# Kernel optimization log

Hardware: AMD Instinct MI355X
Metric: run time of the kernel (lower is better)

Reference implementation:

```python
import jax, jax.numpy as jnp
import numpy as np

B, N, N_MELS = 8, 4096, 64
DIM, LAYERS, HEADS = 256, 4, 4
DIM_HEAD = DIM // HEADS      # 64
INNER = HEADS * DIM_HEAD     # 256
NB_FEAT = 256                # random features
FF_MULT = 4                  # performer_pytorch FeedForward default


def _ortho_projection(rows, cols, rng):
    # gaussian_orthogonal_random_matrix, scaling=0 (performer_pytorch default)
    blocks = []
    for _ in range((rows + cols - 1) // cols):
        q, _ = np.linalg.qr(rng.standard_normal((cols, cols)))
        blocks.append(q.T)
    mat = np.concatenate(blocks)[:rows]
    multiplier = np.linalg.norm(rng.standard_normal((rows, cols)), axis=1)
    return (mat * multiplier[:, None]).astype(np.float32)


def setup_inputs() -> dict:
    rng = np.random.default_rng(0)
    def w(*s, scale=0.02):
        return jnp.asarray(rng.standard_normal(s).astype(np.float32) * scale)
    G2 = 2 * DIM * FF_MULT  # GLU projection width = 2048
    return {
        "x": jnp.asarray(rng.standard_normal((B, N, N_MELS)).astype(np.float32)),
        "proj_w": w(N_MELS, DIM), "proj_b": jnp.zeros((DIM,), jnp.float32),
        "ln1_g": jnp.ones((LAYERS, DIM), jnp.float32), "ln1_b": jnp.zeros((LAYERS, DIM), jnp.float32),
        "wq": w(LAYERS, DIM, INNER), "bq": jnp.zeros((LAYERS, INNER), jnp.float32),
        "wk": w(LAYERS, DIM, INNER), "bk": jnp.zeros((LAYERS, INNER), jnp.float32),
        "wv": w(LAYERS, DIM, INNER), "bv": jnp.zeros((LAYERS, INNER), jnp.float32),
        "wo": w(LAYERS, INNER, DIM), "bo": jnp.zeros((LAYERS, DIM), jnp.float32),
        "ln2_g": jnp.ones((LAYERS, DIM), jnp.float32), "ln2_b": jnp.zeros((LAYERS, DIM), jnp.float32),
        "w1": w(LAYERS, DIM, G2), "b1": jnp.zeros((LAYERS, G2), jnp.float32),
        "w2": w(LAYERS, DIM * FF_MULT, DIM), "b2": jnp.zeros((LAYERS, DIM), jnp.float32),
        "clf_w": w(DIM, 1), "clf_b": jnp.zeros((1,), jnp.float32),
        "proj_mat": jnp.asarray(_ortho_projection(NB_FEAT, DIM_HEAD, rng)),
    }


def _layer_norm(x, g, b, eps=1e-5):
    mu = jnp.mean(x, -1, keepdims=True)
    var = jnp.mean((x - mu) ** 2, -1, keepdims=True)
    return (x - mu) * jax.lax.rsqrt(var + eps) * g + b


def _softmax_kernel(data, proj, is_query, eps=1e-4):
    # FAVOR+ positive random features for softmax (performer_pytorch.softmax_kernel)
    dn = data.shape[-1] ** -0.25          # data_normalizer
    ratio = proj.shape[0] ** -0.5
    dd = jnp.einsum('bhnd,md->bhnm', data * dn, proj)
    diag = jnp.sum(data ** 2, -1, keepdims=True) * 0.5 * (dn ** 2)
    if is_query:
        m = jax.lax.stop_gradient(jnp.max(dd, axis=-1, keepdims=True))
    else:
        m = jax.lax.stop_gradient(jnp.max(dd))
    return ratio * (jnp.exp(dd - diag - m) + eps)


def _split_heads(t):
    b, n, _ = t.shape
    return t.reshape(b, n, HEADS, DIM_HEAD).transpose(0, 2, 1, 3)  # b h n d


def _forward(x, proj_w, proj_b, ln1_g, ln1_b, wq, bq, wk, bk, wv, bv, wo, bo,
             ln2_g, ln2_b, w1, b1, w2, b2, clf_w, clf_b, proj_mat):
    h = x @ proj_w + proj_b                       # [B, N, DIM]
    b, n = h.shape[0], h.shape[1]
    for l in range(LAYERS):
        # --- pre-LN self-attention (FAVOR+, non-causal) ---
        y = _layer_norm(h, ln1_g[l], ln1_b[l])
        q = _split_heads(y @ wq[l] + bq[l])
        k = _split_heads(y @ wk[l] + bk[l])
        v = _split_heads(y @ wv[l] + bv[l])
        qp = _softmax_kernel(q, proj_mat, is_query=True)    # [b,h,n,m]
        kp = _softmax_kernel(k, proj_mat, is_query=False)   # [b,h,n,m]
        d_inv = 1.0 / jnp.einsum('bhnm,bhm->bhn', qp, kp.sum(axis=2))
        ctx = jnp.einsum('bhnm,bhnd->bhmd', kp, v)          # [b,h,m,d]
        o = jnp.einsum('bhmd,bhnm,bhn->bhnd', ctx, qp, d_inv)
        o = o.transpose(0, 2, 1, 3).reshape(b, n, INNER)
        h = h + (o @ wo[l] + bo[l])
        # --- pre-LN GLU feed-forward ---
        y = _layer_norm(h, ln2_g[l], ln2_b[l])
        u = y @ w1[l] + b1[l]
        a, g = jnp.split(u, 2, axis=-1)
        h = h + (jax.nn.gelu(a, approximate=False) * g) @ w2[l] + b2[l]
    # clf: transpose + AdaptiveAvgPool1d(1) == mean over time, then Linear(dim,1)
    pooled = h.mean(axis=1)                       # [B, DIM]
    return (pooled @ clf_w + clf_b)[:, 0]         # [B]


def reference(x, proj_w, proj_b, ln1_g, ln1_b, wq, bq, wk, bk, wv, bv, wo, bo,
              ln2_g, ln2_b, w1, b1, w2, b2, clf_w, clf_b, proj_mat):
    return _forward(x, proj_w, proj_b, ln1_g, ln1_b, wq, bq, wk, bk, wv, bv,
                    wo, bo, ln2_g, ln2_b, w1, b1, w2, b2, clf_w, clf_b, proj_mat)
```

## Files before the change

### kernel.cpp

```cpp
#include <hip/hip_runtime.h>
#include <cstdint>
#include <cstddef>

constexpr float DN = 0.35355339059327373f;
constexpr float RATIO = 0.0625f;
constexpr float EPSF = 1e-4f;

typedef __attribute__((ext_vector_type(8))) short short8;
typedef __attribute__((ext_vector_type(8))) _Float16 half8;
typedef __attribute__((ext_vector_type(4))) float f32x4;

constexpr size_t OFF_H     = 0;
constexpr size_t OFF_YS    = 33554432;
constexpr size_t OFF_WTS   = 50331648;
constexpr size_t OFF_QK    = 67108864;
constexpr size_t OFF_BIG   = 100663296;
constexpr size_t OFF_VT    = 167772160;
constexpr size_t OFF_CTXP  = 188743680;
constexpr size_t OFF_CTXTH = 199229440;
constexpr size_t OFF_CTXTL = 200540160;
constexpr size_t OFF_DIAGQ = 201850880;
constexpr size_t OFF_DIAGK = 202375168;
constexpr size_t OFF_GMAX  = 203423744;
constexpr size_t OFF_POOL  = 203424000;
constexpr size_t OFF_PMTH  = 207749376;
constexpr size_t OFF_PMTL  = 207782144;
constexpr size_t OFF_PWTH  = 207814912;
constexpr size_t OFF_PWTL  = 207847680;
constexpr size_t WS_BYTES  = 207880448;

constexpr size_t WQ_H = 0,       WQ_L = 65536;
constexpr size_t WK_H = 131072,  WK_L = 196608;
constexpr size_t WV_H = 262144,  WV_L = 327680;
constexpr size_t WO_H = 393216,  WO_L = 458752;
constexpr size_t W1_H = 524288,  W1_L = 1048576;
constexpr size_t W2_H = 1572864, W2_L = 1835008;

__device__ __forceinline__ unsigned fkey(float f) {
    unsigned u = __float_as_uint(f);
    return (u & 0x80000000u) ? ~u : (u | 0x80000000u);
}
__device__ __forceinline__ float funkey(unsigned k) {
    unsigned u = (k & 0x80000000u) ? (k ^ 0x80000000u) : ~k;
    return __uint_as_float(u);
}
__device__ __forceinline__ float gelu_exact(float x) {
    return 0.5f * x * (1.0f + erff(x * 0.70710678118654752f));
}
__device__ __forceinline__ void splitf(float x, unsigned short& h, unsigned short& l) {
    unsigned u = __float_as_uint(x);
    unsigned hv = (u + 0x7FFFu + ((u >> 16) & 1)) >> 16;
    h = (unsigned short)hv;
    float lo = x - __uint_as_float(hv << 16);
    unsigned u2 = __float_as_uint(lo);
    l = (unsigned short)((u2 + 0x7FFFu + ((u2 >> 16) & 1)) >> 16);
}
__device__ __forceinline__ unsigned short bf16rne(float x) {
    unsigned u = __float_as_uint(x);
    return (unsigned short)((u + 0x7FFFu + ((u >> 16) & 1)) >> 16);
}
__device__ __forceinline__ unsigned short fp16rne(float x) {
    return __builtin_bit_cast(unsigned short, (_Float16)x);
}
template<bool F16>
__device__ __forceinline__ f32x4 mfma16(short8 a, short8 b, f32x4 c) {
    if constexpr (F16)
        return __builtin_amdgcn_mfma_f32_16x16x32_f16(
            __builtin_bit_cast(half8, a), __builtin_bit_cast(half8, b), c, 0, 0, 0);
    else
        return __builtin_amdgcn_mfma_f32_16x16x32_bf16(a, b, c, 0, 0, 0);
}
__device__ __forceinline__ void xcd_swz(int& bx, int& by) {
    const int gx = gridDim.x;
    const int total = gx * gridDim.y;
    int flat = blockIdx.y * gx + blockIdx.x;
    flat = (flat & 7) * (total >> 3) + (flat >> 3);
    bx = flat % gx; by = flat / gx;
}

#if defined(__has_builtin)
#if __has_builtin(__builtin_amdgcn_global_load_lds)
#define HAVE_GLDS 1
#endif
#endif
__device__ __forceinline__ void glds16(const unsigned short* g, unsigned short* l) {
#ifdef HAVE_GLDS
    __builtin_amdgcn_global_load_lds(
        (const __attribute__((address_space(1))) unsigned int*)g,
        (__attribute__((address_space(3))) unsigned int*)l, 16, 0, 0);
#else
    *(uint4*)l = *(const uint4*)g;
#endif
}

__global__ void fill_sentinel(float* out, int n) {
    int i = threadIdx.x;
    if (i < n) out[i] = 12345.0f;
}
__global__ __launch_bounds__(256) void vt_init(unsigned short* __restrict__ vT, unsigned* __restrict__ gm) {
    int i = blockIdx.x * 256 + threadIdx.x;
    if (i < 4) gm[i] = 0u;
    const int bh = i >> 13;
    const int r = (i >> 9) & 15;
    const unsigned val = (r == 0) ? 0x3C003C00u : 0u;
    uint4 q; q.x = val; q.y = val; q.z = val; q.w = val;
    *(uint4*)(vT + ((size_t)bh * 80 + 64 + r) * 4096 + ((size_t)(i & 511) << 3)) = q;
}

__global__ __launch_bounds__(256) void split_scale(
    const float* __restrict__ src, unsigned short* __restrict__ hi,
    unsigned short* __restrict__ lo, int n, float scale)
{
    int i = blockIdx.x * 256 + threadIdx.x;
    if (i < n) {
        unsigned short h, l;
        splitf(src[i] * scale, h, l);
        hi[i] = h; lo[i] = l;
    }
}

__global__ __launch_bounds__(256) void tofp16_scale(
    const float* __restrict__ src, unsigned short* __restrict__ dst, int n, float scale)
{
    int i = blockIdx.x * 256 + threadIdx.x;
    if (i < n) dst[i] = fp16rne(src[i] * scale);
}

__global__ __launch_bounds__(256) void splitT(
    const float* __restrict__ W, unsigned short* __restrict__ hi,
    unsigned short* __restrict__ lo, int kshift, int N)
{
    int i = blockIdx.x * 256 + threadIdx.x;
    int K = 1 << kshift;
    int n = i >> kshift, k = i & (K - 1);
    unsigned short h, l;
    splitf(W[(size_t)k * N + n], h, l);
    hi[i] = h; lo[i] = l;
}

__global__ __launch_bounds__(256) void split_weights(
    const float* __restrict__ wq, const float* __restrict__ wk,
    const float* __restrict__ wv, const float* __restrict__ wo,
    const float* __restrict__ w1, const float* __restrict__ w2,
    unsigned short* __restrict__ dst)
{
    const int i = blockIdx.x * 256 + threadIdx.x;
    const int lay = i >> 20;
    const int r = i & 1048575;
    float val; size_t oh, ol;
    if (r < 262144) {
        const int m = r >> 16, e = r & 65535;
        const int n = e >> 8, k = e & 255;
        const float* W = (m == 0 ? wq : m == 1 ? wk : m == 2 ? wv : wo);
        val = W[(size_t)lay * 65536 + k * 256 + n];
        oh = (size_t)lay * 2097152 + (size_t)m * 131072 + e;
        ol = oh + 65536;
    } else if (r < 786432) {
        const int e = r - 262144;
        const int n = e >> 8, k = e & 255;
        val = w1[(size_t)lay * 524288 + (size_t)k * 2048 + n];
        oh = (size_t)lay * 2097152 + W1_H + e;
        ol = oh + 524288;
    } else {
        const int e = r - 786432;
        const int n = e >> 10, k = e & 1023;
        val = w2[(size_t)lay * 262144 + (size_t)k * 256 + n];
        oh = (size_t)lay * 2097152 + W2_H + e;
        ol = oh + 262144;
    }
    unsigned short h, l;
    splitf(val, h, l);
    dst[oh] = h; dst[ol] = l;
}

__global__ __launch_bounds__(256) void ln_bf16(
    const float* __restrict__ x, const float* __restrict__ g,
    const float* __restrict__ b, unsigned short* __restrict__ yhi)
{
    const int row = blockIdx.x * 4 + (threadIdx.x >> 6);
    const int lane = threadIdx.x & 63;
    float4 t = *(const float4*)&x[(size_t)row * 256 + lane * 4];
    float s = t.x + t.y + t.z + t.w;
#pragma unroll
    for (int sh = 1; sh < 64; sh <<= 1) s += __shfl_xor(s, sh);
    const float mu = s * (1.0f / 256.0f);
    const float dx = t.x - mu, dy = t.y - mu, dz = t.z - mu, dw = t.w - mu;
    float vv = dx * dx + dy * dy + dz * dz + dw * dw;
#pragma unroll
    for (int sh = 1; sh < 64; sh <<= 1) vv += __shfl_xor(vv, sh);
    const float rstd = rsqrtf(vv * (1.0f / 256.0f) + 1e-5f);
    float4 gv = *(const float4*)&g[lane * 4];
    float4 bv = *(const float4*)&b[lane * 4];
    unsigned short h0 = bf16rne(dx * rstd * gv.x + bv.x);
    unsigned short h1 = bf16rne(dy * rstd * gv.y + bv.y);
    unsigned short h2 = bf16rne(dz * rstd * gv.z + bv.z);
    unsigned short h3 = bf16rne(dw * rstd * gv.w + bv.w);
    uint2 ph;
    ph.x = (unsigned)h0 | ((unsigned)h1 << 16); ph.y = (unsigned)h2 | ((unsigned)h3 << 16);
    *(uint2*)&yhi[(size_t)row * 256 + lane * 4] = ph;
}

template<int EPI, bool ASPLIT, bool BSPLIT, bool F16>
__global__ __launch_bounds__(256) void gemm_mf(
    const unsigned short* __restrict__ Ahi, const unsigned short* __restrict__ Alo, int lda,
    const unsigned short* __restrict__ Bhi, const unsigned short* __restrict__ Blo, int ldb,
    int K,
    const float* __restrict__ bias, const float* __restrict__ res,
    float* __restrict__ C, int ldc,
    unsigned short* __restrict__ Obf,
    const float* __restrict__ diag, unsigned* __restrict__ keys)
{
    constexpr int NP = (ASPLIT ? 2 : 1) + (BSPLIT ? 2 : 1);
    constexpr int PB = ASPLIT ? 2 : 1;
    constexpr int NEED = (EPI == 6) ? 16384 : 0;
    constexpr int LDSN = (NP * 8192 > NEED) ? NP * 8192 : NEED;
    __shared__ unsigned short lds[LDSN];
    __shared__ float red[4];
#define LX(p, h, r, c) lds[(p) * 8192 + (h) * 4096 + (r) * 32 + (c)]
    int bx, by; xcd_swz(bx, by);
    const int tid = threadIdx.x;
    const int m0 = by * 128, n0 = bx * 128;
    const int sr = tid >> 2, sc = (tid & 3) * 8;
    const unsigned short* ga_h = Ahi + (size_t)(m0 + sr) * lda + sc;
    const unsigned short* ga_l = ASPLIT ? (Alo + (size_t)(m0 + sr) * lda + sc) : nullptr;
    const unsigned short* gb_h = Bhi + (size_t)(n0 + sr) * ldb + sc;
    const unsigned short* gb_l = BSPLIT ? (Blo + (size_t)(n0 + sr) * ldb + sc) : nullptr;
    unsigned short* lp = lds + tid * 8;
    const int l = tid & 63, w = tid >> 6;
    const int wr = (w >> 1) * 64, wc = (w & 1) * 64;
    const int fr = l & 15, fq = l >> 4;

    f32x4 acc[4][4];
#pragma unroll
    for (int i = 0; i < 4; ++i)
#pragma unroll
        for (int j = 0; j < 4; ++j) acc[i][j] = (f32x4){0.f, 0.f, 0.f, 0.f};

    for (int k0 = 0; k0 < K; k0 += 64) {
        glds16(ga_h + k0, lp);
        glds16(ga_h + (size_t)64 * lda + k0, lp + 2048);
        glds16(ga_h + k0 + 32, lp + 4096);
        glds16(ga_h + (size_t)64 * lda + k0 + 32, lp + 6144);
        if (ASPLIT) {
            glds16(ga_l + k0, lp + 8192);
            glds16(ga_l + (size_t)64 * lda + k0, lp + 10240);
            glds16(ga_l + k0 + 32, lp + 12288);
            glds16(ga_l + (size_t)64 * lda + k0 + 32, lp + 14336);
        }
        glds16(gb_h + k0, lp + PB * 8192);
        glds16(gb_h + (size_t)64 * ldb + k0, lp + PB * 8192 + 2048);
        glds16(gb_h + k0 + 32, lp + PB * 8192 + 4096);
        glds16(gb_h + (size_t)64 * ldb + k0 + 32, lp + PB * 8192 + 6144);
        if (BSPLIT) {
            glds16(gb_l + k0, lp + (PB + 1) * 8192);
            glds16(gb_l + (size_t)64 * ldb + k0, lp + (PB + 1) * 8192 + 2048);
            glds16(gb_l + k0 + 32, lp + (PB + 1) * 8192 + 4096);
            glds16(gb_l + (size_t)64 * ldb + k0 + 32, lp + (PB + 1) * 8192 + 6144);
        }
        __syncthreads();
#pragma unroll
        for (int h2 = 0; h2 < 2; ++h2) {
            short8 ah[4], al[4];
#pragma unroll
            for (int mf = 0; mf < 4; ++mf) {
                ah[mf] = *(const short8*)&LX(0, h2, wr + mf * 16 + fr, fq * 8);
                if (ASPLIT) al[mf] = *(const short8*)&LX(1, h2, wr + mf * 16 + fr, fq * 8);
            }
#pragma unroll
            for (int nf = 0; nf < 4; ++nf) {
                short8 bh = *(const short8*)&LX(PB, h2, wc + nf * 16 + fr, fq * 8);
#pragma unroll
                for (int mf = 0; mf < 4; ++mf) {
                    acc[mf][nf] = mfma16<F16>(ah[mf], bh, acc[mf][nf]);
                    if (ASPLIT) acc[mf][nf] = mfma16<F16>(al[mf], bh, acc[mf][nf]);
                }
                if (BSPLIT) {
                    short8 bl = *(const short8*)&LX(PB + 1, h2, wc + nf * 16 + fr, fq * 8);
#pragma unroll
                    for (int mf = 0; mf < 4; ++mf)
                        acc[mf][nf] = mfma16<F16>(ah[mf], bl, acc[mf][nf]);
                }
            }
        }
        __syncthreads();
    }

    if constexpr (EPI == 4) {
        float m = -3.4e38f;
#pragma unroll
        for (int mf = 0; mf < 4; ++mf)
#pragma unroll
            for (int nf = 0; nf < 4; ++nf)
#pragma unroll
                for (int v = 0; v < 4; ++v) m = fmaxf(m, acc[mf][nf][v]);
#pragma unroll
        for (int s = 1; s < 64; s <<= 1) m = fmaxf(m, __shfl_xor(m, s));
        if (l == 0) red[w] = m;
        __syncthreads();
        if (tid == 0)
            atomicMax(keys, fkey(fmaxf(fmaxf(red[0], red[1]), fmaxf(red[2], red[3]))));
    } else if constexpr (EPI == 6) {
        const float Mg = funkey(*keys);
        unsigned short* tb = lds;
#pragma unroll
        for (int mf = 0; mf < 4; ++mf)
#pragma unroll
            for (int v = 0; v < 4; ++v) {
                const int rl = wr + mf * 16 + fq * 4 + v;
                const float dg = diag[m0 + rl] + Mg;
#pragma unroll
                for (int nf = 0; nf < 4; ++nf) {
                    const int cl = wc + nf * 16 + fr;
                    const float kv = RATIO * (__expf(acc[mf][nf][v] - dg) + EPSF);
                    tb[rl * 128 + cl] = F16 ? fp16rne(kv) : bf16rne(kv);
                }
            }
        __syncthreads();
        const int tokbase = m0 >> 2;
        const int b = tokbase >> 12, nib = tokbase & 4095;
        const int ml = tid & 127, g2 = tid >> 7;
#pragma unroll
        for (int hh2 = 0; hh2 < 2; ++hh2) {
            const int hh = g2 * 2 + hh2;
            unsigned short* dst = Obf + ((size_t)((b * 4 + hh) * 256 + n0 + ml)) * 4096 + nib;
#pragma unroll
            for (int qq = 0; qq < 4; ++qq) {
                uint4 qv;
                unsigned wv[4];
#pragma unroll
                for (int j = 0; j < 4; ++j) {
                    unsigned s0 = tb[((qq * 8 + j * 2 + 0) * 4 + hh) * 128 + ml];
                    unsigned s1 = tb[((qq * 8 + j * 2 + 1) * 4 + hh) * 128 + ml];
                    wv[j] = s0 | (s1 << 16);
                }
                qv.x = wv[0]; qv.y = wv[1]; qv.z = wv[2]; qv.w = wv[3];
                *(uint4*)(dst + qq * 8) = qv;
            }
        }
    } else {
#pragma unroll
        for (int nf = 0; nf < 4; ++nf) {
            const int col = n0 + wc + nf * 16 + fr;
            float bb = 0.f;
            if (bias != nullptr) bb = bias[col];
#pragma unroll
            for (int mf = 0; mf < 4; ++mf) {
#pragma unroll
                for (int v = 0; v < 4; ++v) {
                    const int row = m0 + wr + mf * 16 + fq * 4 + v;
                    const size_t off = (size_t)row * ldc + col;
                    float val = acc[mf][nf][v] + bb;
                    if (EPI == 1) val += res[off];
                    C[off] = val;
                }
            }
        }
    }
#undef LX
}

__global__ __launch_bounds__(256) void gemm_qkv(
    const unsigned short* __restrict__ A, const unsigned short* __restrict__ wl,
    const float* __restrict__ bq, const float* __restrict__ bk, const float* __restrict__ bv,
    unsigned short* __restrict__ vT, unsigned short* __restrict__ khi,
    unsigned short* __restrict__ qhi, float* __restrict__ diagq, float* __restrict__ diagk)
{
    __shared__ unsigned short lds[24576];
    int bx, by; xcd_swz(bx, by);
    const int sel = by >> 8;
    const int m0 = (by & 255) * 128, n0 = bx * 128;
    const unsigned short* Bh = wl + (sel == 0 ? WV_H : sel == 1 ? WK_H : WQ_H);
    const unsigned short* Bl = wl + (sel == 0 ? WV_L : sel == 1 ? WK_L : WQ_L);
    const float* bias = (sel == 0 ? bv : sel == 1 ? bk : bq);
    const int tid = threadIdx.x;
    const int sr = tid >> 2, sc = (tid & 3) * 8;
    const unsigned short* ga_h = A + (size_t)(m0 + sr) * 256 + sc;
    const unsigned short* gb_h = Bh + (size_t)(n0 + sr) * 256 + sc;
    const unsigned short* gb_l = Bl + (size_t)(n0 + sr) * 256 + sc;
    unsigned short* lp = lds + tid * 8;
    const int l = tid & 63, w = tid >> 6;
    const int wr = (w >> 1) * 64, wc = (w & 1) * 64;
    const int fr = l & 15, fq = l >> 4;

    f32x4 acc[4][4];
#pragma unroll
    for (int i = 0; i < 4; ++i)
#pragma unroll
        for (int j = 0; j < 4; ++j) acc[i][j] = (f32x4){0.f, 0.f, 0.f, 0.f};

    for (int k0 = 0; k0 < 256; k0 += 64) {
        glds16(ga_h + k0, lp);
        glds16(ga_h + (size_t)64 * 256 + k0, lp + 2048);
        glds16(ga_h + k0 + 32, lp + 4096);
        glds16(ga_h + (size_t)64 * 256 + k0 + 32, lp + 6144);
        glds16(gb_h + k0, lp + 8192);
        glds16(gb_h + (size_t)64 * 256 + k0, lp + 10240);
        glds16(gb_h + k0 + 32, lp + 12288);
        glds16(gb_h + (size_t)64 * 256 + k0 + 32, lp + 14336);
        glds16(gb_l + k0, lp + 16384);
        glds16(gb_l + (size_t)64 * 256 + k0, lp + 18432);
        glds16(gb_l + k0 + 32, lp + 20480);
        glds16(gb_l + (size_t)64 * 256 + k0 + 32, lp + 22528);
        __syncthreads();
#pragma unroll
        for (int h2 = 0; h2 < 2; ++h2) {
            short8 ah[4];
#pragma unroll
            for (int mf = 0; mf < 4; ++mf)
                ah[mf] = *(const short8*)&lds[h2 * 4096 + (wr + mf * 16 + fr) * 32 + fq * 8];
#pragma unroll
            for (int nf = 0; nf < 4; ++nf) {
                short8 bh = *(const short8*)&lds[8192 + h2 * 4096 + (wc + nf * 16 + fr) * 32 + fq * 8];
                short8 bl = *(const short8*)&lds[16384 + h2 * 4096 + (wc + nf * 16 + fr) * 32 + fq * 8];
#pragma unroll
                for (int mf = 0; mf < 4; ++mf) {
                    acc[mf][nf] = mfma16<false>(ah[mf], bh, acc[mf][nf]);
                    acc[mf][nf] = mfma16<false>(ah[mf], bl, acc[mf][nf]);
                }
            }
        }
        __syncthreads();
    }

    if (sel == 0) {
        unsigned short* tb = lds;
#pragma unroll
        for (int mf = 0; mf < 4; ++mf)
#pragma unroll
            for (int nf = 0; nf < 4; ++nf) {
                const int cl = wc + nf * 16 + fr;
                const float bb = bias[n0 + cl];
#pragma unroll
                for (int v = 0; v < 4; ++v) {
                    const int rl = wr + mf * 16 + fq * 4 + v;
                    tb[rl * 128 + cl] = fp16rne(acc[mf][nf][v] + bb);
                }
            }
        __syncthreads();
        const int b = m0 >> 12, nib = m0 & 4095;
        const int cl = tid & 127, half = tid >> 7;
        const int ch = n0 + cl, hh = ch >> 6, d = ch & 63;
        unsigned short* dst = vT + ((size_t)((b * 4 + hh) * 80 + d)) * 4096 + nib + half * 64;
#pragma unroll
        for (int qq = 0; qq < 8; ++qq) {
            uint4 qv;
            unsigned wv[4];
#pragma unroll
            for (int j = 0; j < 4; ++j) {
                unsigned s0 = tb[(half * 64 + qq * 8 + j * 2 + 0) * 128 + cl];
                unsigned s1 = tb[(half * 64 + qq * 8 + j * 2 + 1) * 128 + cl];
                wv[j] = s0 | (s1 << 16);
            }
            qv.x = wv[0]; qv.y = wv[1]; qv.z = wv[2]; qv.w = wv[3];
            *(uint4*)(dst + qq * 8) = qv;
        }
    } else {
        float* diag = (sel == 1 ? diagk : diagq);
        unsigned short* Obf = (sel == 1 ? khi : qhi);
        const int head = (n0 + wc) >> 6;
#pragma unroll
        for (int mf = 0; mf < 4; ++mf) {
            float sq[4] = {0.f, 0.f, 0.f, 0.f};
#pragma unroll
            for (int nf = 0; nf < 4; ++nf) {
                const int col = n0 + wc + nf * 16 + fr;
                const float bb = bias[col];
#pragma unroll
                for (int v = 0; v < 4; ++v) {
                    const int row = m0 + wr + mf * 16 + fq * 4 + v;
                    float val = acc[mf][nf][v] + bb;
                    Obf[(size_t)row * 256 + col] = fp16rne(val);
                    sq[v] += val * val;
                }
            }
#pragma unroll
            for (int v = 0; v < 4; ++v) {
                float s = sq[v];
                s += __shfl_xor(s, 1); s += __shfl_xor(s, 2);
                s += __shfl_xor(s, 4); s += __shfl_xor(s, 8);
                if (fr == 0)
                    diag[(size_t)(m0 + wr + mf * 16 + fq * 4 + v) * 4 + head] = s * 0.0625f;
            }
        }
    }
}

__global__ __launch_bounds__(256) void gemm_glu(
    const unsigned short* __restrict__ Ahi,
    const unsigned short* __restrict__ Whi, const unsigned short* __restrict__ Wlo,
    const float* __restrict__ b1, unsigned short* __restrict__ Obf)
{
    __shared__ unsigned short ldsA[8192];
    __shared__ unsigned short ldsB[16384];
    int bx, by; xcd_swz(bx, by);
    const int tid = threadIdx.x;
    const int m0 = by * 128, p0 = bx * 64;
    const int sr = tid >> 2, sc = (tid & 3) * 8;
    const unsigned short* ga  = Ahi + (size_t)(m0 + sr) * 256 + sc;
    const unsigned short* gb0 = Whi + (size_t)(p0 + sr) * 256 + sc;
    const unsigned short* gb1 = Wlo + (size_t)(p0 + sr) * 256 + sc;
    const unsigned short* gb2 = Whi + (size_t)(1024 + p0 + sr) * 256 + sc;
    const unsigned short* gb3 = Wlo + (size_t)(1024 + p0 + sr) * 256 + sc;
    unsigned short* lpA = ldsA + tid * 8;
    unsigned short* lpB = ldsB + tid * 8;
    const int l = tid & 63, w = tid >> 6;
    const int wr = (w >> 1) * 64, wc = (w & 1) * 32;
    const int fr = l & 15, fq = l >> 4;

    f32x4 aa[4][2], ag[4][2];
#pragma unroll
    for (int i = 0; i < 4; ++i)
#pragma unroll
        for (int j = 0; j < 2; ++j) {
            aa[i][j] = (f32x4){0.f, 0.f, 0.f, 0.f};
            ag[i][j] = (f32x4){0.f, 0.f, 0.f, 0.f};
        }

    for (int k0 = 0; k0 < 256; k0 += 64) {
        glds16(ga + k0, lpA);
        glds16(ga + 64 * 256 + k0, lpA + 2048);
        glds16(ga + k0 + 32, lpA + 4096);
        glds16(ga + 64 * 256 + k0 + 32, lpA + 6144);
        glds16(gb0 + k0, lpB);
        glds16(gb0 + k0 + 32, lpB + 2048);
        glds16(gb1 + k0, lpB + 4096);
        glds16(gb1 + k0 + 32, lpB + 6144);
        glds16(gb2 + k0, lpB + 8192);
        glds16(gb2 + k0 + 32, lpB + 10240);
        glds16(gb3 + k0, lpB + 12288);
        glds16(gb3 + k0 + 32, lpB + 14336);
        __syncthreads();
#pragma unroll
        for (int h2 = 0; h2 < 2; ++h2) {
            short8 ah[4];
#pragma unroll
            for (int mf = 0; mf < 4; ++mf)
                ah[mf] = *(const short8*)&ldsA[h2 * 4096 + (wr + mf * 16 + fr) * 32 + fq * 8];
#pragma unroll
            for (int nf = 0; nf < 2; ++nf) {
                const int br_ = h2 * 2048 + (wc + nf * 16 + fr) * 32 + fq * 8;
                short8 bah = *(const short8*)&ldsB[br_];
                short8 bal = *(const short8*)&ldsB[4096 + br_];
                short8 bgh = *(const short8*)&ldsB[8192 + br_];
                short8 bgl = *(const short8*)&ldsB[12288 + br_];
#pragma unroll
                for (int mf = 0; mf < 4; ++mf) {
                    aa[mf][nf] = mfma16<false>(ah[mf], bah, aa[mf][nf]);
                    aa[mf][nf] = mfma16<false>(ah[mf], bal, aa[mf][nf]);
                    ag[mf][nf] = mfma16<false>(ah[mf], bgh, ag[mf][nf]);
                    ag[mf][nf] = mfma16<false>(ah[mf], bgl, ag[mf][nf]);
                }
            }
        }
        __syncthreads();
    }
#pragma unroll
    for (int nf = 0; nf < 2; ++nf) {
        const int ch = p0 + wc + nf * 16 + fr;
        const float ba = b1[ch], bg = b1[1024 + ch];
#pragma unroll
        for (int mf = 0; mf < 4; ++mf) {
#pragma unroll
            for (int v = 0; v < 4; ++v) {
                const int row = m0 + wr + mf * 16 + fq * 4 + v;
                float u = aa[mf][nf][v] + ba, g = ag[mf][nf][v] + bg;
                Obf[(size_t)row * 1024 + ch] = bf16rne(gelu_exact(u) * g);
            }
        }
    }
}

__global__ __launch_bounds__(256) void ctx_mfma(
    const unsigned short* __restrict__ kpT, const unsigned short* __restrict__ vT,
    float* __restrict__ ctxp)
{
    __shared__ unsigned short la[4096];
    __shared__ unsigned short lb[5120];
    int bx, by; xcd_swz(bx, by);
    const int bh = by, mt = bx & 3, kc = bx >> 2;
    const int tid = threadIdx.x;
    const int l = tid & 63, w = tid >> 6;
    const int wr = w * 16, fr = l & 15, fq = l >> 4;
    const int sr = tid >> 2, sc = (tid & 3) * 8;
    const unsigned short* ga  = kpT + ((size_t)bh * 256 + mt * 64 + sr) * 4096 + kc * 1024 + sc;
    const unsigned short* gb  = vT + ((size_t)bh * 80 + sr) * 4096 + kc * 1024 + sc;
    const unsigned short* gb2 = vT + ((size_t)bh * 80 + 64 + sr) * 4096 + kc * 1024 + sc;

    f32x4 acc[5];
#pragma unroll
    for (int j = 0; j < 5; ++j) acc[j] = (f32x4){0.f, 0.f, 0.f, 0.f};

    for (int k0 = 0; k0 < 1024; k0 += 64) {
        glds16(ga + k0, la + tid * 8);
        glds16(ga + k0 + 32, la + 2048 + tid * 8);
        glds16(gb + k0, lb + tid * 8);
        glds16(gb + k0 + 32, lb + 2560 + tid * 8);
        if (tid < 64) {
            glds16(gb2 + k0, lb + 2048 + tid * 8);
            glds16(gb2 + k0 + 32, lb + 2560 + 2048 + tid * 8);
        }
        __syncthreads();
#pragma unroll
        for (int h2 = 0; h2 < 2; ++h2) {
            short8 av = *(const short8*)&la[h2 * 2048 + (wr + fr) * 32 + fq * 8];
#pragma unroll
            for (int nf = 0; nf < 5; ++nf) {
                short8 bv = *(const short8*)&lb[h2 * 2560 + (nf * 16 + fr) * 32 + fq * 8];
                acc[nf] = mfma16<true>(av, bv, acc[nf]);
            }
        }
        __syncthreads();
    }
#pragma unroll
    for (int v = 0; v < 4; ++v) {
        const int row = mt * 64 + wr + fq * 4 + v;
#pragma unroll
        for (int nf = 0; nf < 5; ++nf)
            ctxp[((size_t)(kc * 32 + bh) * 256 + row) * 80 + nf * 16 + fr] = acc[nf][v];
    }
}

__global__ __launch_bounds__(256) void ctx_fix(
    const float* __restrict__ ctxp, unsigned short* __restrict__ cth)
{
    __shared__ float s[64][81];
    const int m0 = blockIdx.x * 64, bh = blockIdx.y;
    const int tid = threadIdx.x;
    for (int i = tid; i < 5120; i += 256) {
        const int ml = i / 80, dc = i % 80;
        float sum = 0.f;
#pragma unroll
        for (int kc = 0; kc < 4; ++kc)
            sum += ctxp[((size_t)(kc * 32 + bh) * 256 + m0 + ml) * 80 + dc];
        s[ml][dc] = sum;
    }
    __syncthreads();
    for (int i = tid; i < 5120; i += 256) {
        const int dc = i >> 6, ml = i & 63;
        cth[((size_t)bh * 80 + dc) * 256 + m0 + ml] = fp16rne(s[ml][dc]);
    }
}

__global__ __launch_bounds__(256) void qo_mfma(
    const unsigned short* __restrict__ qhi, const unsigned short* __restrict__ pmh,
    const unsigned short* __restrict__ cth, const float* __restrict__ diagq,
    unsigned short* __restrict__ osh)
{
    __shared__ unsigned short lds[16384 + 2560];
    __shared__ float rmax4[64][4];
    int bx, by; xcd_swz(bx, by);
    const int bh = by, b = bh >> 2, hh = bh & 3;
    const int t0 = bx * 64;
    const int tid = threadIdx.x;
    const int l = tid & 63, w = tid >> 6;
    const int fr = l & 15, fq = l >> 4;

    const int wc1 = w * 64;
    f32x4 a1[4][4];
#pragma unroll
    for (int i = 0; i < 4; ++i)
#pragma unroll
        for (int j = 0; j < 4; ++j) a1[i][j] = (f32x4){0.f, 0.f, 0.f, 0.f};

    const unsigned short* gq = qhi + (size_t)(b * 4096 + t0) * 256 + hh * 64;
#pragma unroll
    for (int ks = 0; ks < 2; ++ks) {
        const int k0 = ks * 32;
        glds16(gq + (size_t)(tid >> 2) * 256 + k0 + (tid & 3) * 8, lds + tid * 8);
#pragma unroll
        for (int i2 = 0; i2 < 4; ++i2) {
            const int c = tid + i2 * 256;
            glds16(pmh + (size_t)(c >> 2) * 64 + k0 + (c & 3) * 8, lds + 2048 + c * 8);
        }
        __syncthreads();
        short8 av[4];
#pragma unroll
        for (int mf = 0; mf < 4; ++mf)
            av[mf] = *(const short8*)&lds[(mf * 16 + fr) * 32 + fq * 8];
#pragma unroll
        for (int nf = 0; nf < 4; ++nf) {
            short8 bh_ = *(const short8*)&lds[2048 + (wc1 + nf * 16 + fr) * 32 + fq * 8];
#pragma unroll
            for (int mf = 0; mf < 4; ++mf)
                a1[mf][nf] = mfma16<true>(av[mf], bh_, a1[mf][nf]);
        }
        __syncthreads();
    }
#pragma unroll
    for (int mf = 0; mf < 4; ++mf)
#pragma unroll
        for (int v = 0; v < 4; ++v) {
            float rm = a1[mf][0][v];
#pragma unroll
            for (int nf = 1; nf < 4; ++nf) rm = fmaxf(rm, a1[mf][nf][v]);
            rm = fmaxf(rm, __shfl_xor(rm, 1));
            rm = fmaxf(rm, __shfl_xor(rm, 2));
            rm = fmaxf(rm, __shfl_xor(rm, 4));
            rm = fmaxf(rm, __shfl_xor(rm, 8));
            if (fr == 0) rmax4[mf * 16 + fq * 4 + v][w] = rm;
        }
    __syncthreads();
#pragma unroll
    for (int mf = 0; mf < 4; ++mf)
#pragma unroll
        for (int v = 0; v < 4; ++v) {
            const int tok = mf * 16 + fq * 4 + v;
            const float dg = diagq[(size_t)(b * 4096 + t0 + tok) * 4 + hh]
                           + fmaxf(fmaxf(rmax4[tok][0], rmax4[tok][1]),
                                   fmaxf(rmax4[tok][2], rmax4[tok][3]));
#pragma unroll
            for (int nf = 0; nf < 4; ++nf) {
                const int m = wc1 + nf * 16 + fr;
                lds[tok * 256 + (m ^ ((tok & 7) << 3))] =
                    fp16rne(RATIO * (__expf(a1[mf][nf][v] - dg) + EPSF));
            }
        }
    __syncthreads();

    unsigned short* lds2 = lds + 16384;
    f32x4 a2[5];
#pragma unroll
    for (int j = 0; j < 5; ++j) a2[j] = (f32x4){0.f, 0.f, 0.f, 0.f};
    const size_t bbase = (size_t)bh * 80 * 256;

    for (int k0 = 0; k0 < 256; k0 += 32) {
        glds16(cth + bbase + (size_t)(tid >> 2) * 256 + k0 + (tid & 3) * 8, lds2 + tid * 8);
        if (tid < 64) {
            const int c = 256 + tid;
            glds16(cth + bbase + (size_t)(c >> 2) * 256 + k0 + (c & 3) * 8, lds2 + c * 8);
        }
        __syncthreads();
        const int tok = w * 16 + fr;
        const int c = ((k0 >> 3) + fq) ^ (tok & 7);
        short8 av = *(const short8*)&lds[tok * 256 + c * 8];
#pragma unroll
        for (int nf = 0; nf < 5; ++nf) {
            short8 bvh = *(const short8*)&lds2[(nf * 16 + fr) * 32 + fq * 8];
            a2[nf] = mfma16<true>(av, bvh, a2[nf]);
        }
        __syncthreads();
    }
#pragma unroll
    for (int v = 0; v < 4; ++v) {
        const float den = __shfl(a2[4][v], (int)(l & 48));
        const float dinv = 1.0f / den;
        const int tok = w * 16 + fq * 4 + v;
        const size_t obase = (size_t)(b * 4096 + t0 + tok) * 256 + hh * 64;
#pragma unroll
        for (int nf = 0; nf < 4; ++nf)
            osh[obase + nf * 16 + fr] = bf16rne(a2[nf][v] * dinv);
    }
}

__global__ __launch_bounds__(256) void pool1_kernel(const float* __restrict__ h, float* __restrict__ part)
{
    const int b = blockIdx.x >> 4, ch = blockIdx.x & 15;
    const int tid = threadIdx.x;
    float acc = 0.f;
    for (int n = 0; n < 256; ++n)
        acc += h[((size_t)(b * 4096 + ch * 256 + n)) * 256 + tid];
    part[(size_t)blockIdx.x * 256 + tid] = acc;
}

__global__ __launch_bounds__(256) void pool2_kernel(
    const float* __restrict__ part, const float* __restrict__ cw,
    const float* __restrict__ cb, float* __restrict__ out)
{
    const int b = blockIdx.x, tid = threadIdx.x;
    float acc = 0.f;
#pragma unroll
    for (int c = 0; c < 16; ++c) acc += part[(size_t)(b * 16 + c) * 256 + tid];
    float val = acc * (1.0f / 4096.0f) * cw[tid];
#pragma unroll
    for (int s = 1; s < 64; s <<= 1) val += __shfl_xor(val, s);
    __shared__ float red[4];
    if ((tid & 63) == 0) red[tid >> 6] = val;
    __syncthreads();
    if (tid == 0) out[b] = red[0] + red[1] + red[2] + red[3] + cb[0];
}

extern "C" void kernel_launch(void* const* d_in, const int* in_sizes, int n_in,
                              void* d_out, int out_size, void* d_ws, size_t ws_size,
                              hipStream_t stream)
{
    (void)in_sizes; (void)n_in;
    if (ws_size < WS_BYTES) {
        fill_sentinel<<<1, 64, 0, stream>>>((float*)d_out, out_size);
        return;
    }

    const float* x     = (const float*)d_in[0];
    const float* projw = (const float*)d_in[1];
    const float* projb = (const float*)d_in[2];
    const float* ln1g  = (const float*)d_in[3];
    const float* ln1b  = (const float*)d_in[4];
    const float* wq    = (const float*)d_in[5];
    const float* bq    = (const float*)d_in[6];
    const float* wk    = (const float*)d_in[7];
    const float* bk    = (const float*)d_in[8];
    const float* wv    = (const float*)d_in[9];
    const float* bv    = (const float*)d_in[10];
    const float* wo    = (const float*)d_in[11];
    const float* bo    = (const float*)d_in[12];
    const float* ln2g  = (const float*)d_in[13];
    const float* ln2b  = (const float*)d_in[14];
    const float* w1    = (const float*)d_in[15];
    const float* b1    = (const float*)d_in[16];
    const float* w2    = (const float*)d_in[17];
    const float* b2    = (const float*)d_in[18];
    const float* clfw  = (const float*)d_in[19];
    const float* clfb  = (const float*)d_in[20];
    const float* projm = (const float*)d_in[21];

    char* WS = (char*)d_ws;
    float* h            = (float*)(WS + OFF_H);
    unsigned short* ysh = (unsigned short*)(WS + OFF_YS);
    unsigned short* wts = (unsigned short*)(WS + OFF_WTS);
    unsigned short* khi = (unsigned short*)(WS + OFF_QK);
    unsigned short* qhi = khi + 8388608;
    unsigned short* big = (unsigned short*)(WS + OFF_BIG);
    unsigned short* vT  = (unsigned short*)(WS + OFF_VT);
    float* ctxp         = (float*)(WS + OFF_CTXP);
    unsigned short* cth = (unsigned short*)(WS + OFF_CTXTH);
    float* diagq        = (float*)(WS + OFF_DIAGQ);
    float* diagk        = (float*)(WS + OFF_DIAGK);
    unsigned* gmax      = (unsigned*)(WS + OFF_GMAX);
    float* pool         = (float*)(WS + OFF_POOL);
    unsigned short* pmt_h = (unsigned short*)(WS + OFF_PMTH);
    unsigned short* pwt_h = (unsigned short*)(WS + OFF_PWTH);
    unsigned short* pwt_l = (unsigned short*)(WS + OFF_PWTL);
    unsigned short* xsh = big;
    unsigned short* xsl = big + 2097152;
    unsigned short* kpT = big;
    unsigned short* ffb = big;
    unsigned short* osh = ysh;

    split_scale<<<8192, 256, 0, stream>>>(x, xsh, xsl, 2097152, 1.0f);
    splitT<<<64, 256, 0, stream>>>(projw, pwt_h, pwt_l, 6, 256);
    tofp16_scale<<<64, 256, 0, stream>>>(projm, pmt_h, 16384, DN);
    vt_init<<<1024, 256, 0, stream>>>(vT, gmax);
    split_weights<<<16384, 256, 0, stream>>>(wq, wk, wv, wo, w1, w2, wts);
    gemm_mf<0, true, true, false><<<dim3(2, 256), 256, 0, stream>>>(xsh, xsl, 64,
        pwt_h, pwt_l, 64, 64, projb, nullptr, h, 256, nullptr, nullptr, nullptr);

    for (int l = 0; l < 4; ++l) {
        unsigned short* wl = wts + (size_t)l * 2097152;

        ln_bf16<<<8192, 256, 0, stream>>>(h, ln1g + l * 256, ln1b + l * 256, ysh);
        gemm_qkv<<<dim3(2, 768), 256, 0, stream>>>(ysh, wl,
            bq + l * 256, bk + l * 256, bv + l * 256, vT, khi, qhi, diagq, diagk);
        gemm_mf<4, false, false, true><<<dim3(2, 1024), 256, 0, stream>>>(khi, nullptr, 64,
            pmt_h, nullptr, 64, 64, nullptr, nullptr, nullptr, 256, nullptr, nullptr, gmax + l);
        gemm_mf<6, false, false, true><<<dim3(2, 1024), 256, 0, stream>>>(khi, nullptr, 64,
            pmt_h, nullptr, 64, 64, nullptr, nullptr, nullptr, 256, kpT, diagk, gmax + l);
        ctx_mfma<<<dim3(16, 32), 256, 0, stream>>>(kpT, vT, ctxp);
        ctx_fix<<<dim3(4, 32), 256, 0, stream>>>(ctxp, cth);
        qo_mfma<<<dim3(64, 32), 256, 0, stream>>>(qhi, pmt_h, cth, diagq, osh);
        gemm_mf<1, false, true, false><<<dim3(2, 256), 256, 0, stream>>>(osh, nullptr, 256,
            wl + WO_H, wl + WO_L, 256, 256, bo + l * 256, h, h, 256, nullptr, nullptr, nullptr);

        ln_bf16<<<8192, 256, 0, stream>>>(h, ln2g + l * 256, ln2b + l * 256, ysh);
        gemm_glu<<<dim3(16, 256), 256, 0, stream>>>(ysh, wl + W1_H, wl + W1_L,
            b1 + (size_t)l * 2048, ffb);
        gemm_mf<1, false, true, false><<<dim3(2, 256), 256, 0, stream>>>(ffb, nullptr, 1024,
            wl + W2_H, wl + W2_L, 1024, 1024, b2 + l * 256, h, h, 256, nullptr, nullptr, nullptr);
    }

    pool1_kernel<<<128, 256, 0, stream>>>(h, pool);
    pool2_kernel<<<8, 256, 0, stream>>>(pool, clfw, clfb, (float*)d_out);
}
```

Measured before the change: 1.341 ms.

## Switch per-layer GEMMs from split bf16 hi/lo weights to single fp16

Weights are now stored as one fp16 copy instead of a bf16 hi/lo pair. Activations (layernorm output, GLU output, attention output) are also written in fp16. The QKV, GLU, out-projection and FFN-down GEMMs each run a single fp16 MFMA per tile instead of two bf16 MFMAs, which roughly halves matrix-core work, weight traffic and LDS use in those kernels. The cost is accuracy: fp16 has fewer exponent bits and drops the lo correction term, so results may drift from the fp32 reference.

```diff
diff --git a/kernel.cpp b/kernel.cpp
--- a/kernel.cpp
+++ b/kernel.cpp
@@ -18,23 +18,21 @@
 constexpr size_t OFF_VT    = 167772160;
 constexpr size_t OFF_CTXP  = 188743680;
 constexpr size_t OFF_CTXTH = 199229440;
-constexpr size_t OFF_CTXTL = 200540160;
 constexpr size_t OFF_DIAGQ = 201850880;
 constexpr size_t OFF_DIAGK = 202375168;
 constexpr size_t OFF_GMAX  = 203423744;
 constexpr size_t OFF_POOL  = 203424000;
 constexpr size_t OFF_PMTH  = 207749376;
-constexpr size_t OFF_PMTL  = 207782144;
 constexpr size_t OFF_PWTH  = 207814912;
 constexpr size_t OFF_PWTL  = 207847680;
 constexpr size_t WS_BYTES  = 207880448;
 
-constexpr size_t WQ_H = 0,       WQ_L = 65536;
-constexpr size_t WK_H = 131072,  WK_L = 196608;
-constexpr size_t WV_H = 262144,  WV_L = 327680;
-constexpr size_t WO_H = 393216,  WO_L = 458752;
-constexpr size_t W1_H = 524288,  W1_L = 1048576;
-constexpr size_t W2_H = 1572864, W2_L = 1835008;
+constexpr size_t WQF = 0;
+constexpr size_t WKF = 65536;
+constexpr size_t WVF = 131072;
+constexpr size_t WOF = 196608;
+constexpr size_t W1F = 262144;
+constexpr size_t W2F = 786432;
 
 __device__ __forceinline__ unsigned fkey(float f) {
     unsigned u = __float_as_uint(f);
@@ -147,33 +145,28 @@
     const int i = blockIdx.x * 256 + threadIdx.x;
     const int lay = i >> 20;
     const int r = i & 1048575;
-    float val; size_t oh, ol;
+    float val; size_t oh;
     if (r < 262144) {
         const int m = r >> 16, e = r & 65535;
         const int n = e >> 8, k = e & 255;
         const float* W = (m == 0 ? wq : m == 1 ? wk : m == 2 ? wv : wo);
         val = W[(size_t)lay * 65536 + k * 256 + n];
-        oh = (size_t)lay * 2097152 + (size_t)m * 131072 + e;
-        ol = oh + 65536;
+        oh = (size_t)lay * 1048576 + (size_t)m * 65536 + e;
     } else if (r < 786432) {
         const int e = r - 262144;
         const int n = e >> 8, k = e & 255;
         val = w1[(size_t)lay * 524288 + (size_t)k * 2048 + n];
-        oh = (size_t)lay * 2097152 + W1_H + e;
-        ol = oh + 524288;
+        oh = (size_t)lay * 1048576 + W1F + e;
     } else {
         const int e = r - 786432;
         const int n = e >> 10, k = e & 1023;
         val = w2[(size_t)lay * 262144 + (size_t)k * 256 + n];
-        oh = (size_t)lay * 2097152 + W2_H + e;
-        ol = oh + 262144;
-    }
-    unsigned short h, l;
-    splitf(val, h, l);
-    dst[oh] = h; dst[ol] = l;
-}
-
-__global__ __launch_bounds__(256) void ln_bf16(
+        oh = (size_t)lay * 1048576 + W2F + e;
+    }
+    dst[oh] = fp16rne(val);
+}
+
+__global__ __launch_bounds__(256) void ln_f16(
     const float* __restrict__ x, const float* __restrict__ g,
     const float* __restrict__ b, unsigned short* __restrict__ yhi)
 {
@@ -191,10 +184,10 @@
     const float rstd = rsqrtf(vv * (1.0f / 256.0f) + 1e-5f);
     float4 gv = *(const float4*)&g[lane * 4];
     float4 bv = *(const float4*)&b[lane * 4];
-    unsigned short h0 = bf16rne(dx * rstd * gv.x + bv.x);
-    unsigned short h1 = bf16rne(dy * rstd * gv.y + bv.y);
-    unsigned short h2 = bf16rne(dz * rstd * gv.z + bv.z);
-    unsigned short h3 = bf16rne(dw * rstd * gv.w + bv.w);
+    unsigned short h0 = fp16rne(dx * rstd * gv.x + bv.x);
+    unsigned short h1 = fp16rne(dy * rstd * gv.y + bv.y);
+    unsigned short h2 = fp16rne(dz * rstd * gv.z + bv.z);
+    unsigned short h3 = fp16rne(dw * rstd * gv.w + bv.w);
     uint2 ph;
     ph.x = (unsigned)h0 | ((unsigned)h1 << 16); ph.y = (unsigned)h2 | ((unsigned)h3 << 16);
     *(uint2*)&yhi[(size_t)row * 256 + lane * 4] = ph;
@@ -311,8 +304,7 @@
 #pragma unroll
                 for (int nf = 0; nf < 4; ++nf) {
                     const int cl = wc + nf * 16 + fr;
-                    const float kv = RATIO * (__expf(acc[mf][nf][v] - dg) + EPSF);
-                    tb[rl * 128 + cl] = F16 ? fp16rne(kv) : bf16rne(kv);
+                    tb[rl * 128 + cl] = fp16rne(RATIO * (__expf(acc[mf][nf][v] - dg) + EPSF));
                 }
             }
         __syncthreads();
@@ -365,18 +357,16 @@
     unsigned short* __restrict__ vT, unsigned short* __restrict__ khi,
     unsigned short* __restrict__ qhi, float* __restrict__ diagq, float* __restrict__ diagk)
 {
-    __shared__ unsigned short lds[24576];
+    __shared__ unsigned short lds[16384];
     int bx, by; xcd_swz(bx, by);
     const int sel = by >> 8;
     const int m0 = (by & 255) * 128, n0 = bx * 128;
-    const unsigned short* Bh = wl + (sel == 0 ? WV_H : sel == 1 ? WK_H : WQ_H);
-    const unsigned short* Bl = wl + (sel == 0 ? WV_L : sel == 1 ? WK_L : WQ_L);
+    const unsigned short* Bw = wl + (sel == 0 ? WVF : sel == 1 ? WKF : WQF);
     const float* bias = (sel == 0 ? bv : sel == 1 ? bk : bq);
     const int tid = threadIdx.x;
     const int sr = tid >> 2, sc = (tid & 3) * 8;
-    const unsigned short* ga_h = A + (size_t)(m0 + sr) * 256 + sc;
-    const unsigned short* gb_h = Bh + (size_t)(n0 + sr) * 256 + sc;
-    const unsigned short* gb_l = Bl + (size_t)(n0 + sr) * 256 + sc;
+    const unsigned short* ga = A + (size_t)(m0 + sr) * 256 + sc;
+    const unsigned short* gb = Bw + (size_t)(n0 + sr) * 256 + sc;
     unsigned short* lp = lds + tid * 8;
     const int l = tid & 63, w = tid >> 6;
     const int wr = (w >> 1) * 64, wc = (w & 1) * 64;
@@ -389,18 +379,14 @@
         for (int j = 0; j < 4; ++j) acc[i][j] = (f32x4){0.f, 0.f, 0.f, 0.f};
 
     for (int k0 = 0; k0 < 256; k0 += 64) {
-        glds16(ga_h + k0, lp);
-        glds16(ga_h + (size_t)64 * 256 + k0, lp + 2048);
-        glds16(ga_h + k0 + 32, lp + 4096);
-        glds16(ga_h + (size_t)64 * 256 + k0 + 32, lp + 6144);
-        glds16(gb_h + k0, lp + 8192);
-        glds16(gb_h + (size_t)64 * 256 + k0, lp + 10240);
-        glds16(gb_h + k0 + 32, lp + 12288);
-        glds16(gb_h + (size_t)64 * 256 + k0 + 32, lp + 14336);
-        glds16(gb_l + k0, lp + 16384);
-        glds16(gb_l + (size_t)64 * 256 + k0, lp + 18432);
-        glds16(gb_l + k0 + 32, lp + 20480);
-        glds16(gb_l + (size_t)64 * 256 + k0 + 32, lp + 22528);
+        glds16(ga + k0, lp);
+        glds16(ga + (size_t)64 * 256 + k0, lp + 2048);
+        glds16(ga + k0 + 32, lp + 4096);
+        glds16(ga + (size_t)64 * 256 + k0 + 32, lp + 6144);
+        glds16(gb + k0, lp + 8192);
+        glds16(gb + (size_t)64 * 256 + k0, lp + 10240);
+        glds16(gb + k0 + 32, lp + 12288);
+        glds16(gb + (size_t)64 * 256 + k0 + 32, lp + 14336);
         __syncthreads();
 #pragma unroll
         for (int h2 = 0; h2 < 2; ++h2) {
@@ -411,12 +397,9 @@
 #pragma unroll
             for (int nf = 0; nf < 4; ++nf) {
                 short8 bh = *(const short8*)&lds[8192 + h2 * 4096 + (wc + nf * 16 + fr) * 32 + fq * 8];
-                short8 bl = *(const short8*)&lds[16384 + h2 * 4096 + (wc + nf * 16 + fr) * 32 + fq * 8];
-#pragma unroll
-                for (int mf = 0; mf < 4; ++mf) {
-                    acc[mf][nf] = mfma16<false>(ah[mf], bh, acc[mf][nf]);
-                    acc[mf][nf] = mfma16<false>(ah[mf], bl, acc[mf][nf]);
-                }
+#pragma unroll
+                for (int mf = 0; mf < 4; ++mf)
+                    acc[mf][nf] = mfma16<true>(ah[mf], bh, acc[mf][nf]);
             }
         }
         __syncthreads();
@@ -486,21 +469,18 @@
 }
 
 __global__ __launch_bounds__(256) void gemm_glu(
-    const unsigned short* __restrict__ Ahi,
-    const unsigned short* __restrict__ Whi, const unsigned short* __restrict__ Wlo,
+    const unsigned short* __restrict__ Ahi, const unsigned short* __restrict__ Wf,
     const float* __restrict__ b1, unsigned short* __restrict__ Obf)
 {
     __shared__ unsigned short ldsA[8192];
-    __shared__ unsigned short ldsB[16384];
+    __shared__ unsigned short ldsB[8192];
     int bx, by; xcd_swz(bx, by);
     const int tid = threadIdx.x;
     const int m0 = by * 128, p0 = bx * 64;
     const int sr = tid >> 2, sc = (tid & 3) * 8;
     const unsigned short* ga  = Ahi + (size_t)(m0 + sr) * 256 + sc;
-    const unsigned short* gb0 = Whi + (size_t)(p0 + sr) * 256 + sc;
-    const unsigned short* gb1 = Wlo + (size_t)(p0 + sr) * 256 + sc;
-    const unsigned short* gb2 = Whi + (size_t)(1024 + p0 + sr) * 256 + sc;
-    const unsigned short* gb3 = Wlo + (size_t)(1024 + p0 + sr) * 256 + sc;
+    const unsigned short* gba = Wf + (size_t)(p0 + sr) * 256 + sc;
+    const unsigned short* gbg = Wf + (size_t)(1024 + p0 + sr) * 256 + sc;
     unsigned short* lpA = ldsA + tid * 8;
     unsigned short* lpB = ldsB + tid * 8;
     const int l = tid & 63, w = tid >> 6;
@@ -521,14 +501,10 @@
         glds16(ga + 64 * 256 + k0, lpA + 2048);
         glds16(ga + k0 + 32, lpA + 4096);
         glds16(ga + 64 * 256 + k0 + 32, lpA + 6144);
-        glds16(gb0 + k0, lpB);
-        glds16(gb0 + k0 + 32, lpB + 2048);
-        glds16(gb1 + k0, lpB + 4096);
-        glds16(gb1 + k0 + 32, lpB + 6144);
-        glds16(gb2 + k0, lpB + 8192);
-        glds16(gb2 + k0 + 32, lpB + 10240);
-        glds16(gb3 + k0, lpB + 12288);
-        glds16(gb3 + k0 + 32, lpB + 14336);
+        glds16(gba + k0, lpB);
+        glds16(gba + k0 + 32, lpB + 2048);
+        glds16(gbg + k0, lpB + 4096);
+        glds16(gbg + k0 + 32, lpB + 6144);
         __syncthreads();
 #pragma unroll
         for (int h2 = 0; h2 < 2; ++h2) {
@@ -539,16 +515,12 @@
 #pragma unroll
             for (int nf = 0; nf < 2; ++nf) {
                 const int br_ = h2 * 2048 + (wc + nf * 16 + fr) * 32 + fq * 8;
-                short8 bah = *(const short8*)&ldsB[br_];
-                short8 bal = *(const short8*)&ldsB[4096 + br_];
-                short8 bgh = *(const short8*)&ldsB[8192 + br_];
-                short8 bgl = *(const short8*)&ldsB[12288 + br_];
+                short8 bva = *(const short8*)&ldsB[br_];
+                short8 bvg = *(const short8*)&ldsB[4096 + br_];
 #pragma unroll
                 for (int mf = 0; mf < 4; ++mf) {
-                    aa[mf][nf] = mfma16<false>(ah[mf], bah, aa[mf][nf]);
-                    aa[mf][nf] = mfma16<false>(ah[mf], bal, aa[mf][nf]);
-                    ag[mf][nf] = mfma16<false>(ah[mf], bgh, ag[mf][nf]);
-                    ag[mf][nf] = mfma16<false>(ah[mf], bgl, ag[mf][nf]);
+                    aa[mf][nf] = mfma16<true>(ah[mf], bva, aa[mf][nf]);
+                    ag[mf][nf] = mfma16<true>(ah[mf], bvg, ag[mf][nf]);
                 }
             }
         }
@@ -564,7 +536,7 @@
             for (int v = 0; v < 4; ++v) {
                 const int row = m0 + wr + mf * 16 + fq * 4 + v;
                 float u = aa[mf][nf][v] + ba, g = ag[mf][nf][v] + bg;
-                Obf[(size_t)row * 1024 + ch] = bf16rne(gelu_exact(u) * g);
+                Obf[(size_t)row * 1024 + ch] = fp16rne(gelu_exact(u) * g);
             }
         }
     }
@@ -748,7 +720,7 @@
         const size_t obase = (size_t)(b * 4096 + t0 + tok) * 256 + hh * 64;
 #pragma unroll
         for (int nf = 0; nf < 4; ++nf)
-            osh[obase + nf * 16 + fr] = bf16rne(a2[nf][v] * dinv);
+            osh[obase + nf * 16 + fr] = fp16rne(a2[nf][v] * dinv);
     }
 }
 
@@ -844,9 +816,9 @@
         pwt_h, pwt_l, 64, 64, projb, nullptr, h, 256, nullptr, nullptr, nullptr);
 
     for (int l = 0; l < 4; ++l) {
-        unsigned short* wl = wts + (size_t)l * 2097152;
-
-        ln_bf16<<<8192, 256, 0, stream>>>(h, ln1g + l * 256, ln1b + l * 256, ysh);
+        unsigned short* wl = wts + (size_t)l * 1048576;
+
+        ln_f16<<<8192, 256, 0, stream>>>(h, ln1g + l * 256, ln1b + l * 256, ysh);
         gemm_qkv<<<dim3(2, 768), 256, 0, stream>>>(ysh, wl,
             bq + l * 256, bk + l * 256, bv + l * 256, vT, khi, qhi, diagq, diagk);
         gemm_mf<4, false, false, true><<<dim3(2, 1024), 256, 0, stream>>>(khi, nullptr, 64,
@@ -856,14 +828,14 @@
         ctx_mfma<<<dim3(16, 32), 256, 0, stream>>>(kpT, vT, ctxp);
         ctx_fix<<<dim3(4, 32), 256, 0, stream>>>(ctxp, cth);
         qo_mfma<<<dim3(64, 32), 256, 0, stream>>>(qhi, pmt_h, cth, diagq, osh);
-        gemm_mf<1, false, true, false><<<dim3(2, 256), 256, 0, stream>>>(osh, nullptr, 256,
-            wl + WO_H, wl + WO_L, 256, 256, bo + l * 256, h, h, 256, nullptr, nullptr, nullptr);
-
-        ln_bf16<<<8192, 256, 0, stream>>>(h, ln2g + l * 256, ln2b + l * 256, ysh);
-        gemm_glu<<<dim3(16, 256), 256, 0, stream>>>(ysh, wl + W1_H, wl + W1_L,
+        gemm_mf<1, false, false, true><<<dim3(2, 256), 256, 0, stream>>>(osh, nullptr, 256,
+            wl + WOF, nullptr, 256, 256, bo + l * 256, h, h, 256, nullptr, nullptr, nullptr);
+
+        ln_f16<<<8192, 256, 0, stream>>>(h, ln2g + l * 256, ln2b + l * 256, ysh);
+        gemm_glu<<<dim3(16, 256), 256, 0, stream>>>(ysh, wl + W1F,
             b1 + (size_t)l * 2048, ffb);
-        gemm_mf<1, false, true, false><<<dim3(2, 256), 256, 0, stream>>>(ffb, nullptr, 1024,
-            wl + W2_H, wl + W2_L, 1024, 1024, b2 + l * 256, h, h, 256, nullptr, nullptr, nullptr);
+        gemm_mf<1, false, false, true><<<dim3(2, 256), 256, 0, stream>>>(ffb, nullptr, 1024,
+            wl + W2F, nullptr, 1024, 1024, b2 + l * 256, h, h, 256, nullptr, nullptr, nullptr);
     }
 
     pool1_kernel<<<128, 256, 0, stream>>>(h, pool);
```

Result: faster. 1.173 ms (-12.5%).
